# Kernel optimization log

Hardware: AMD Instinct MI355X
Metric: run time of the kernel (lower is better)

Reference implementation:

```python
import jax, jax.numpy as jnp
import numpy as np


def setup_inputs() -> dict:
    key = jax.random.key(0)
    ks = jax.random.split(key, 10)
    B, T, C, E, H, W = 32, 768, 448, 256, 56, 56
    s = 0.02  # param init scale
    return {
        "text_feature": jax.random.normal(ks[0], (B, T), jnp.float32),
        "image_feature": jax.random.normal(ks[1], (B, C, H, W), jnp.float32),
        "q_w": jax.random.normal(ks[2], (E, T), jnp.float32) * s,
        "q_b": jax.random.normal(ks[3], (E,), jnp.float32) * s,
        "k_w": jax.random.normal(ks[4], (E, C), jnp.float32) * s,
        "k_b": jax.random.normal(ks[5], (E,), jnp.float32) * s,
        "v_w": jax.random.normal(ks[6], (E, C), jnp.float32) * s,
        "v_b": jax.random.normal(ks[7], (E,), jnp.float32) * s,
        "o_w": jax.random.normal(ks[8], (C, E), jnp.float32) * s,
        "o_b": jax.random.normal(ks[9], (C,), jnp.float32) * s,
    }


def reference(text_feature, image_feature, q_w, q_b, k_w, k_b, v_w, v_b, o_w, o_b):
    B, C, H, W = image_feature.shape
    E = q_w.shape[0]
    # query: Linear(text_dim -> embed_dim)  -> [B, E]
    q = text_feature @ q_w.T + q_b
    # key/value: 1x1 conv == per-pixel linear over channels -> [B, E, H*W]
    img = image_feature.reshape(B, C, H * W)          # [B, C, N]
    k = jnp.einsum("ec,bcn->ben", k_w, img) + k_b[None, :, None]
    v = jnp.einsum("ec,bcn->ben", v_w, img) + v_b[None, :, None]
    # single-query attention over spatial positions
    scale = 1.0 / jnp.sqrt(jnp.asarray(E, image_feature.dtype))
    attn = jax.nn.softmax(jnp.einsum("be,ben->bn", q, k) * scale, axis=-1)  # [B, N]
    pooled = jnp.einsum("bn,ben->be", attn, v)        # [B, E]
    # output 1x1 conv on a spatially-constant map == linear once, then broadcast
    out = pooled @ o_w.T + o_b                        # [B, C]
    return image_feature + out[:, :, None, None]
```

## Files before the change

kernel.cpp:

```cpp
#include <hip/hip_runtime.h>
#include <math.h>

#define B_  32
#define T_  768
#define C_  448
#define E_  256
#define N_  3136
#define N4_ 784
#define NTILE_ 16
#define NT4_ 49
#define TOTAL4_ 11239424

__global__ __launch_bounds__(256) void kA_qk(
    const float* __restrict__ text, const float* __restrict__ q_w,
    const float* __restrict__ q_b,  const float* __restrict__ k_w,
    float* __restrict__ qk)
{
    const int b = blockIdx.x, tid = threadIdx.x;
    __shared__ float t_lds[T_];
    __shared__ float q_lds[E_];
    for (int i = tid; i < T_; i += 256) t_lds[i] = text[b * T_ + i];
    __syncthreads();
    {
        const int e = tid;
        float acc = q_b[e];
        const float* qw = q_w + (size_t)e * T_;
        #pragma unroll 8
        for (int t = 0; t < T_; ++t) acc = fmaf(t_lds[t], qw[t], acc);
        q_lds[e] = acc;
    }
    __syncthreads();
    const float scale = 0.0625f;
    for (int c = tid; c < C_; c += 256) {
        float acc = 0.f;
        #pragma unroll 4
        for (int e = 0; e < E_; ++e) acc = fmaf(q_lds[e], k_w[e * C_ + c], acc);
        qk[b * C_ + c] = acc * scale;
    }
}

__global__ __launch_bounds__(256) void kB_logits_pool(
    const float* __restrict__ img, const float* __restrict__ qk,
    float* __restrict__ Ppart,
    float* __restrict__ msloc)
{
    const int t = blockIdx.x;
    const int b = blockIdx.y;
    const int tid = threadIdx.x;
    const int w = tid >> 6, lane = tid & 63;

    __shared__ float  qk_lds[C_];
    __shared__ float4 plog[4][NT4_];
    __shared__ float4 w_lds[NT4_];

    for (int c = tid; c < C_; c += 256) qk_lds[c] = qk[b * C_ + c];
    __syncthreads();

    const float4* imgb = (const float4*)img + (size_t)(b * C_) * N4_ + t * NT4_;

    const int c0 = w * 112;
    if (lane < NT4_) {
        float4 acc = {0.f, 0.f, 0.f, 0.f};
        #pragma unroll 4
        for (int k = 0; k < 112; ++k) {
            const float qkc = qk_lds[c0 + k];
            const float4 x = imgb[(size_t)(c0 + k) * N4_ + lane];
            acc.x = fmaf(qkc, x.x, acc.x); acc.y = fmaf(qkc, x.y, acc.y);
            acc.z = fmaf(qkc, x.z, acc.z); acc.w = fmaf(qkc, x.w, acc.w);
        }
        plog[w][lane] = acc;
    }
    __syncthreads();

    if (w == 0) {
        float4 l4;
        float m = -1e30f;
        if (lane < NT4_) {
            l4 = plog[0][lane];
            const float4 p1 = plog[1][lane], p2 = plog[2][lane], p3 = plog[3][lane];
            l4.x += p1.x + p2.x + p3.x; l4.y += p1.y + p2.y + p3.y;
            l4.z += p1.z + p2.z + p3.z; l4.w += p1.w + p2.w + p3.w;
            m = fmaxf(fmaxf(l4.x, l4.y), fmaxf(l4.z, l4.w));
        }
        for (int off = 32; off; off >>= 1) m = fmaxf(m, __shfl_xor(m, off));
        float s = 0.f;
        if (lane < NT4_) {
            float4 e4;
            e4.x = expf(l4.x - m); e4.y = expf(l4.y - m);
            e4.z = expf(l4.z - m); e4.w = expf(l4.w - m);
            w_lds[lane] = e4;
            s = e4.x + e4.y + e4.z + e4.w;
        }
        for (int off = 32; off; off >>= 1) s += __shfl_xor(s, off);
        if (lane == 0) {
            msloc[(b * NTILE_ + t) * 2 + 0] = m;
            msloc[(b * NTILE_ + t) * 2 + 1] = s;
        }
    }
    __syncthreads();

    #pragma unroll 2
    for (int k = 0; k < 112; ++k) {
        const int c = c0 + k;
        float p = 0.f;
        if (lane < NT4_) {
            const float4 x  = imgb[(size_t)c * N4_ + lane];
            const float4 ww = w_lds[lane];
            p = ww.x * x.x + ww.y * x.y + ww.z * x.z + ww.w * x.w;
        }
        for (int off = 32; off; off >>= 1) p += __shfl_xor(p, off);
        if (lane == 0) Ppart[((size_t)b * NTILE_ + t) * C_ + c] = p;
    }
}

__global__ __launch_bounds__(256) void kC_combine(
    const float* __restrict__ Ppart, const float* __restrict__ msloc,
    const float* __restrict__ v_w,   const float* __restrict__ v_b,
    const float* __restrict__ o_w,   const float* __restrict__ o_b,
    float* __restrict__ outvec)
{
    const int b = blockIdx.x, tid = threadIdx.x;
    __shared__ float p_lds[C_];
    __shared__ float e_lds[E_];
    __shared__ float scl[NTILE_];
    __shared__ float invD_sh;

    if (tid == 0) {
        float M = -1e30f;
        for (int t = 0; t < NTILE_; ++t)
            M = fmaxf(M, msloc[(b * NTILE_ + t) * 2]);
        float D = 0.f;
        for (int t = 0; t < NTILE_; ++t) {
            const float e = expf(msloc[(b * NTILE_ + t) * 2] - M);
            scl[t] = e;
            D = fmaf(msloc[(b * NTILE_ + t) * 2 + 1], e, D);
        }
        invD_sh = 1.f / D;
    }
    __syncthreads();
    const float invD = invD_sh;

    for (int c = tid; c < C_; c += 256) {
        float s = 0.f;
        #pragma unroll
        for (int t = 0; t < NTILE_; ++t)
            s = fmaf(Ppart[((size_t)b * NTILE_ + t) * C_ + c], scl[t], s);
        p_lds[c] = s * invD;
    }
    __syncthreads();
    {
        const int e = tid;
        float acc = v_b[e];
        const float* vw = v_w + (size_t)e * C_;
        #pragma unroll 4
        for (int c = 0; c < C_; ++c) acc = fmaf(vw[c], p_lds[c], acc);
        e_lds[e] = acc;
    }
    __syncthreads();
    for (int c = tid; c < C_; c += 256) {
        float acc = o_b[c];
        const float* ow = o_w + (size_t)c * E_;
        #pragma unroll 4
        for (int e = 0; e < E_; ++e) acc = fmaf(ow[e], e_lds[e], acc);
        outvec[b * C_ + c] = acc;
    }
}

__global__ __launch_bounds__(256) void kD_add(
    const float* __restrict__ img, const float* __restrict__ outvec,
    float* __restrict__ out)
{
    const unsigned i = blockIdx.x * 256u + threadIdx.x;
    const float4 x = ((const float4*)img)[i];
    const float o = outvec[i / N4_];
    float4 r;
    r.x = x.x + o; r.y = x.y + o; r.z = x.z + o; r.w = x.w + o;
    ((float4*)out)[i] = r;
}

extern "C" void kernel_launch(void* const* d_in, const int* in_sizes, int n_in,
                              void* d_out, int out_size, void* d_ws, size_t ws_size,
                              hipStream_t stream) {
    const float* text = (const float*)d_in[0];
    const float* img  = (const float*)d_in[1];
    const float* q_w  = (const float*)d_in[2];
    const float* q_b  = (const float*)d_in[3];
    const float* k_w  = (const float*)d_in[4];
    const float* k_b  = (const float*)d_in[5];
    const float* v_w  = (const float*)d_in[6];
    const float* v_b  = (const float*)d_in[7];
    const float* o_w  = (const float*)d_in[8];
    const float* o_b  = (const float*)d_in[9];
    float* out = (float*)d_out;
    (void)k_b; (void)in_sizes; (void)n_in; (void)out_size; (void)ws_size;

    float* ws     = (float*)d_ws;
    float* qk     = ws;
    float* Ppart  = qk + B_ * C_;
    float* msloc  = Ppart + B_ * NTILE_ * C_;
    float* outvec = msloc + B_ * NTILE_ * 2;

    kA_qk<<<B_, 256, 0, stream>>>(text, q_w, q_b, k_w, qk);
    kB_logits_pool<<<dim3(NTILE_, B_), 256, 0, stream>>>(img, qk, Ppart, msloc);
    kC_combine<<<B_, 256, 0, stream>>>(Ppart, msloc, v_w, v_b, o_w, o_b, outvec);
    kD_add<<<TOTAL4_ / 256, 256, 0, stream>>>(img, outvec, out);
}
```

Measured before the change: 534.2 us.

## Retile logits/pool kernel into 49 spatial tiles with 16x16 thread layout

```diff
diff --git a/kernel.cpp b/kernel.cpp
--- a/kernel.cpp
+++ b/kernel.cpp
@@ -7,8 +7,7 @@
 #define E_  256
 #define N_  3136
 #define N4_ 784
-#define NTILE_ 16
-#define NT4_ 49
+#define NT_ 49
 #define TOTAL4_ 11239424
 
 __global__ __launch_bounds__(256) void kA_qk(
@@ -44,72 +43,60 @@
     float* __restrict__ Ppart,
     float* __restrict__ msloc)
 {
-    const int t = blockIdx.x;
-    const int b = blockIdx.y;
+    const int nt = blockIdx.x;
+    const int b  = blockIdx.y;
     const int tid = threadIdx.x;
-    const int w = tid >> 6, lane = tid & 63;
+    const int cg  = tid >> 4;
+    const int n4  = tid & 15;
 
-    __shared__ float  qk_lds[C_];
-    __shared__ float4 plog[4][NT4_];
-    __shared__ float4 w_lds[NT4_];
+    __shared__ float qk_lds[C_];
+    __shared__ float partf[16 * 64];
+    __shared__ float w_lds[64];
 
     for (int c = tid; c < C_; c += 256) qk_lds[c] = qk[b * C_ + c];
     __syncthreads();
 
-    const float4* imgb = (const float4*)img + (size_t)(b * C_) * N4_ + t * NT4_;
+    const float4* imgb = (const float4*)img + (size_t)(b * C_) * N4_ + nt * 16;
 
-    const int c0 = w * 112;
-    if (lane < NT4_) {
-        float4 acc = {0.f, 0.f, 0.f, 0.f};
-        #pragma unroll 4
-        for (int k = 0; k < 112; ++k) {
-            const float qkc = qk_lds[c0 + k];
-            const float4 x = imgb[(size_t)(c0 + k) * N4_ + lane];
-            acc.x = fmaf(qkc, x.x, acc.x); acc.y = fmaf(qkc, x.y, acc.y);
-            acc.z = fmaf(qkc, x.z, acc.z); acc.w = fmaf(qkc, x.w, acc.w);
-        }
-        plog[w][lane] = acc;
+    float4 acc = {0.f, 0.f, 0.f, 0.f};
+    #pragma unroll 4
+    for (int i = 0; i < 28; ++i) {
+        const int c = i * 16 + cg;
+        const float w = qk_lds[c];
+        const float4 x = imgb[(size_t)c * N4_ + n4];
+        acc.x = fmaf(w, x.x, acc.x); acc.y = fmaf(w, x.y, acc.y);
+        acc.z = fmaf(w, x.z, acc.z); acc.w = fmaf(w, x.w, acc.w);
     }
+    ((float4*)partf)[cg * 16 + n4] = acc;
     __syncthreads();
 
-    if (w == 0) {
-        float4 l4;
-        float m = -1e30f;
-        if (lane < NT4_) {
-            l4 = plog[0][lane];
-            const float4 p1 = plog[1][lane], p2 = plog[2][lane], p3 = plog[3][lane];
-            l4.x += p1.x + p2.x + p3.x; l4.y += p1.y + p2.y + p3.y;
-            l4.z += p1.z + p2.z + p3.z; l4.w += p1.w + p2.w + p3.w;
-            m = fmaxf(fmaxf(l4.x, l4.y), fmaxf(l4.z, l4.w));
-        }
+    if (tid < 64) {
+        const int n = tid;
+        float l = 0.f;
+        #pragma unroll
+        for (int g = 0; g < 16; ++g) l += partf[g * 64 + n];
+        float m = l;
         for (int off = 32; off; off >>= 1) m = fmaxf(m, __shfl_xor(m, off));
-        float s = 0.f;
-        if (lane < NT4_) {
-            float4 e4;
-            e4.x = expf(l4.x - m); e4.y = expf(l4.y - m);
-            e4.z = expf(l4.z - m); e4.w = expf(l4.w - m);
-            w_lds[lane] = e4;
-            s = e4.x + e4.y + e4.z + e4.w;
-        }
+        const float e = expf(l - m);
+        float s = e;
         for (int off = 32; off; off >>= 1) s += __shfl_xor(s, off);
-        if (lane == 0) {
-            msloc[(b * NTILE_ + t) * 2 + 0] = m;
-            msloc[(b * NTILE_ + t) * 2 + 1] = s;
+        w_lds[n] = e;
+        if (n == 0) {
+            msloc[(b * NT_ + nt) * 2 + 0] = m;
+            msloc[(b * NT_ + nt) * 2 + 1] = s;
         }
     }
     __syncthreads();
 
-    #pragma unroll 2
-    for (int k = 0; k < 112; ++k) {
-        const int c = c0 + k;
-        float p = 0.f;
-        if (lane < NT4_) {
-            const float4 x  = imgb[(size_t)c * N4_ + lane];
-            const float4 ww = w_lds[lane];
-            p = ww.x * x.x + ww.y * x.y + ww.z * x.z + ww.w * x.w;
-        }
-        for (int off = 32; off; off >>= 1) p += __shfl_xor(p, off);
-        if (lane == 0) Ppart[((size_t)b * NTILE_ + t) * C_ + c] = p;
+    const float4 w4 = ((const float4*)w_lds)[n4];
+    #pragma unroll 4
+    for (int i = 0; i < 28; ++i) {
+        const int c = i * 16 + cg;
+        const float4 x = imgb[(size_t)c * N4_ + n4];
+        float p = w4.x * x.x + w4.y * x.y + w4.z * x.z + w4.w * x.w;
+        p += __shfl_xor(p, 1); p += __shfl_xor(p, 2);
+        p += __shfl_xor(p, 4); p += __shfl_xor(p, 8);
+        if (n4 == 0) Ppart[((size_t)b * NT_ + nt) * C_ + c] = p;
     }
 }
 
@@ -122,29 +109,28 @@
     const int b = blockIdx.x, tid = threadIdx.x;
     __shared__ float p_lds[C_];
     __shared__ float e_lds[E_];
-    __shared__ float scl[NTILE_];
+    __shared__ float scl[NT_];
     __shared__ float invD_sh;
 
-    if (tid == 0) {
-        float M = -1e30f;
-        for (int t = 0; t < NTILE_; ++t)
-            M = fmaxf(M, msloc[(b * NTILE_ + t) * 2]);
-        float D = 0.f;
-        for (int t = 0; t < NTILE_; ++t) {
-            const float e = expf(msloc[(b * NTILE_ + t) * 2] - M);
-            scl[t] = e;
-            D = fmaf(msloc[(b * NTILE_ + t) * 2 + 1], e, D);
-        }
-        invD_sh = 1.f / D;
+    if (tid < 64) {
+        const bool ok = (tid < NT_);
+        const float m = ok ? msloc[(b * NT_ + tid) * 2 + 0] : -1e30f;
+        float M = m;
+        for (int off = 32; off; off >>= 1) M = fmaxf(M, __shfl_xor(M, off));
+        const float e = ok ? expf(m - M) : 0.f;
+        float d = ok ? msloc[(b * NT_ + tid) * 2 + 1] * e : 0.f;
+        for (int off = 32; off; off >>= 1) d += __shfl_xor(d, off);
+        if (ok) scl[tid] = e;
+        if (tid == 0) invD_sh = 1.f / d;
     }
     __syncthreads();
     const float invD = invD_sh;
 
     for (int c = tid; c < C_; c += 256) {
         float s = 0.f;
-        #pragma unroll
-        for (int t = 0; t < NTILE_; ++t)
-            s = fmaf(Ppart[((size_t)b * NTILE_ + t) * C_ + c], scl[t], s);
+        #pragma unroll 7
+        for (int t = 0; t < NT_; ++t)
+            s = fmaf(Ppart[((size_t)b * NT_ + t) * C_ + c], scl[t], s);
         p_lds[c] = s * invD;
     }
     __syncthreads();
@@ -197,11 +183,11 @@
     float* ws     = (float*)d_ws;
     float* qk     = ws;
     float* Ppart  = qk + B_ * C_;
-    float* msloc  = Ppart + B_ * NTILE_ * C_;
-    float* outvec = msloc + B_ * NTILE_ * 2;
+    float* msloc  = Ppart + B_ * NT_ * C_;
+    float* outvec = msloc + B_ * NT_ * 2;
 
     kA_qk<<<B_, 256, 0, stream>>>(text, q_w, q_b, k_w, qk);
-    kB_logits_pool<<<dim3(NTILE_, B_), 256, 0, stream>>>(img, qk, Ppart, msloc);
+    kB_logits_pool<<<dim3(NT_, B_), 256, 0, stream>>>(img, qk, Ppart, msloc);
     kC_combine<<<B_, 256, 0, stream>>>(Ppart, msloc, v_w, v_b, o_w, o_b, outvec);
     kD_add<<<TOTAL4_ / 256, 256, 0, stream>>>(img, outvec, out);
 }
```

New measurement: 503.2 us. 1.06x faster.
